# Optimization experiments

Measured on AMD Instinct MI355X. Metric: run time of the kernel, lower is better.

Reference implementation:

```python
import jax, jax.numpy as jnp
import numpy as np

D_MODEL = 1024
D_STATE = 16
D_CONV = 4
EXPAND = 2
D_INNER = D_MODEL * EXPAND


def setup_inputs() -> dict:
    key = jax.random.key(0)
    ks = jax.random.split(key, 10)
    B, L = 2, 2048
    x = jax.random.normal(ks[0], (B, L, D_MODEL), jnp.float32)
    W_in = jax.random.normal(ks[1], (2 * D_INNER, D_MODEL), jnp.float32) * (1.0 / np.sqrt(D_MODEL))
    conv_w = jax.random.normal(ks[2], (D_INNER, 1, D_CONV), jnp.float32) * (1.0 / np.sqrt(D_CONV))
    conv_b = jax.random.normal(ks[3], (D_INNER,), jnp.float32) * 0.1
    W_x = jax.random.normal(ks[4], (2 * D_STATE + 1, D_INNER), jnp.float32) * (1.0 / np.sqrt(D_INNER))
    A_log = jnp.log(jnp.abs(jax.random.normal(ks[5], (D_INNER, D_STATE), jnp.float32)) + 1e-4)
    D_param = jnp.ones((D_INNER,), jnp.float32)
    W_dt = jax.random.normal(ks[6], (D_INNER, 1), jnp.float32)
    b_dt = jax.random.normal(ks[7], (D_INNER,), jnp.float32) * 0.1
    W_out = jax.random.normal(ks[8], (D_MODEL, D_INNER), jnp.float32) * (1.0 / np.sqrt(D_INNER))
    return {"x": x, "W_in": W_in, "conv_w": conv_w, "conv_b": conv_b, "W_x": W_x,
            "A_log": A_log, "D_param": D_param, "W_dt": W_dt, "b_dt": b_dt, "W_out": W_out}


def _forward(x, W_in, conv_w, conv_b, W_x, A_log, D_param, W_dt, b_dt, W_out):
    B, L, _ = x.shape
    xz = x @ W_in.T                                  # [B,L,2*d_inner]
    x_ssm, z = jnp.split(xz, 2, axis=-1)
    # causal depthwise conv: torch pads both sides d_conv-1 then truncates to L == left-pad only
    xc = jnp.transpose(x_ssm, (0, 2, 1))             # [B,d_inner,L]
    xc = jax.lax.conv_general_dilated(
        xc, conv_w, window_strides=(1,), padding=[(D_CONV - 1, 0)],
        feature_group_count=D_INNER, dimension_numbers=("NCH", "OIH", "NCH"))
    xc = xc + conv_b[None, :, None]
    x_ssm = jax.nn.silu(jnp.transpose(xc, (0, 2, 1)))  # [B,L,d_inner]
    proj = x_ssm @ W_x.T                              # [B,L,2*d_state+1]
    B_ssm = proj[..., :D_STATE]                       # [B,L,d_state]
    C_ssm = proj[..., D_STATE:2 * D_STATE]            # [B,L,d_state]
    dt = jax.nn.softplus(proj[..., -1:] * W_dt[:, 0] + b_dt)  # [B,L,d_inner]
    A = -jnp.exp(A_log)                               # [d_inner,d_state]

    def step(h, inp):
        dt_t, Bt, Ct, xt = inp                        # [B,d_inner],[B,n],[B,n],[B,d_inner]
        dA = jnp.exp(dt_t[..., None] * A)             # [B,d_inner,d_state]
        h = dA * h + (xt * dt_t)[..., None] * Bt[:, None, :]
        y = jnp.einsum("bdn,bn->bd", h, Ct)
        return h, y

    h0 = jnp.zeros((B, D_INNER, D_STATE), x.dtype)
    inputs = (jnp.transpose(dt, (1, 0, 2)), jnp.transpose(B_ssm, (1, 0, 2)),
              jnp.transpose(C_ssm, (1, 0, 2)), jnp.transpose(x_ssm, (1, 0, 2)))
    _, ys = jax.lax.scan(step, h0, inputs)            # ys: [L,B,d_inner]
    y = jnp.transpose(ys, (1, 0, 2)) + x_ssm * D_param
    y = y * jax.nn.silu(z)
    return y @ W_out.T


def reference(x, W_in, conv_w, conv_b, W_x, A_log, D_param, W_dt, b_dt, W_out):
    return _forward(x, W_in, conv_w, conv_b, W_x, A_log, D_param, W_dt, b_dt, W_out)
```

## Files before the change

kernel.cpp:

```cpp
#include <hip/hip_runtime.h>
#include <hip/hip_bf16.h>
#include <cstddef>

#define DMODEL 1024
#define DI     2048
#define DS     16
#define LSEQ   2048
#define BATCH  2
#define NC     128
#define TCH    (LSEQ / NC)

typedef __attribute__((ext_vector_type(8))) short short8;
typedef __attribute__((ext_vector_type(4))) float f32x4;
typedef __attribute__((ext_vector_type(2))) float f32x2;
typedef __attribute__((ext_vector_type(8))) unsigned short us8;

__device__ __forceinline__ unsigned short f2bf(float f) {
    unsigned int u = __float_as_uint(f);
    unsigned int r = (u + 0x7fff + ((u >> 16) & 1)) >> 16;
    return (unsigned short)r;
}
__device__ __forceinline__ float bf2f(unsigned short b) {
    return __uint_as_float(((unsigned int)b) << 16);
}

__device__ __forceinline__ float fexp2(float x) {
#if __has_builtin(__builtin_amdgcn_exp2f)
    return __builtin_amdgcn_exp2f(x);
#else
    return exp2f(x);
#endif
}
__device__ __forceinline__ float flog2(float x) {
#if __has_builtin(__builtin_amdgcn_logf)
    return __builtin_amdgcn_logf(x);
#else
    return log2f(x);
#endif
}

#define LOG2E 1.4426950408889634f
#define RLOG2E 0.6931471805599453f

__device__ __forceinline__ float softplus_f(float v) {
    return (v > 20.f) ? v : flog2(1.f + fexp2(v * LOG2E)) * RLOG2E;
}

__device__ __forceinline__ void gload_lds16(const void* g, void* l) {
    __builtin_amdgcn_global_load_lds(
        (const __attribute__((address_space(1))) unsigned int*)g,
        (__attribute__((address_space(3))) unsigned int*)l, 16, 0, 0);
}

__global__ void cvt_bf16(const float* __restrict__ in, unsigned short* __restrict__ out, int n8) {
    int i = blockIdx.x * 256 + threadIdx.x;
    if (i >= n8) return;
    const float4* p = reinterpret_cast<const float4*>(in) + i * 2;
    float4 v0 = p[0], v1 = p[1];
    us8 o;
    o[0] = f2bf(v0.x); o[1] = f2bf(v0.y); o[2] = f2bf(v0.z); o[3] = f2bf(v0.w);
    o[4] = f2bf(v1.x); o[5] = f2bf(v1.y); o[6] = f2bf(v1.z); o[7] = f2bf(v1.w);
    *reinterpret_cast<us8*>(out + (size_t)i * 8) = o;
}

__global__ void prep_wx(const float* __restrict__ wx, unsigned short* __restrict__ out) {
    int i = blockIdx.x * 256 + threadIdx.x;
    if (i >= 48 * 2048 / 8) return;
    size_t o = (size_t)i * 8;
    int row = (int)(o >> 11);
    us8 v;
    if (row < 33) {
        const float4* p = reinterpret_cast<const float4*>(wx + o);
        float4 v0 = p[0], v1 = p[1];
        v[0] = f2bf(v0.x); v[1] = f2bf(v0.y); v[2] = f2bf(v0.z); v[3] = f2bf(v0.w);
        v[4] = f2bf(v1.x); v[5] = f2bf(v1.y); v[6] = f2bf(v1.z); v[7] = f2bf(v1.w);
    } else {
        v = (us8)0;
    }
    *reinterpret_cast<us8*>(out + o) = v;
}

__global__ void prep_A(const float* __restrict__ A_log, float* __restrict__ At2) {
    int i = blockIdx.x * 256 + threadIdx.x;
    if (i >= DS * DI) return;
    int n = i / DI, d = i % DI;
    At2[i] = -__expf(A_log[d * DS + n]) * LOG2E;
}

#define NT1 32
__global__ __launch_bounds__(512, 1)
void gemm1_pipe(const unsigned short* __restrict__ A, const unsigned short* __restrict__ B,
                unsigned short* __restrict__ C) {
    __shared__ unsigned short lds[4][2][256 * 32];

    const int tid = threadIdx.x;
    const int wid = tid >> 6, ln = tid & 63;
    const int wm = wid >> 2, wn = wid & 3;

    int wg = blockIdx.x;
    wg = (wg & 7) * 32 + (wg >> 3);
    const int m0 = (wg >> 4) * 256;
    const int n0 = (wg & 15) * 256;

    const int srow = tid >> 2;
    const int sun  = tid & 3;
    const int ksrc = ((sun ^ ((srow >> 1) & 3)) * 8);

    const int fr = ln & 15;
    const int fku = (ln >> 4);

    f32x4 acc[8][4] = {};

    #define STAGE1(kt)                                                                     \
        do {                                                                               \
            const int bq_ = (kt) & 3;                                                      \
            gload_lds16(A + (size_t)(m0 + srow) * 1024 + (kt) * 32 + ksrc,                 \
                        &lds[bq_][0][srow * 32 + sun * 8]);                                \
            gload_lds16(A + (size_t)(m0 + 128 + srow) * 1024 + (kt) * 32 + ksrc,           \
                        &lds[bq_][0][(128 + srow) * 32 + sun * 8]);                        \
            gload_lds16(B + (size_t)(n0 + srow) * 1024 + (kt) * 32 + ksrc,                 \
                        &lds[bq_][1][srow * 32 + sun * 8]);                                \
            gload_lds16(B + (size_t)(n0 + 128 + srow) * 1024 + (kt) * 32 + ksrc,           \
                        &lds[bq_][1][(128 + srow) * 32 + sun * 8]);                        \
        } while (0)

    STAGE1(0); STAGE1(1); STAGE1(2);
    asm volatile("s_waitcnt vmcnt(8)" ::: "memory");
    __builtin_amdgcn_s_barrier();
    __builtin_amdgcn_sched_barrier(0);

    for (int kt = 0; kt < NT1; ++kt) {
        const int bq = kt & 3;
        if (kt + 3 < NT1) STAGE1(kt + 3);

        short8 af_lo[4], bfr[4], af_hi[4];
        #pragma unroll
        for (int i = 0; i < 4; ++i) {
            int r = wm * 128 + i * 16 + fr;
            int u = fku ^ ((r >> 1) & 3);
            af_lo[i] = *reinterpret_cast<const short8*>(&lds[bq][0][r * 32 + u * 8]);
        }
        #pragma unroll
        for (int j = 0; j < 4; ++j) {
            int r = wn * 64 + j * 16 + fr;
            int u = fku ^ ((r >> 1) & 3);
            bfr[j] = *reinterpret_cast<const short8*>(&lds[bq][1][r * 32 + u * 8]);
        }
        #pragma unroll
        for (int i = 0; i < 4; ++i) {
            int r = wm * 128 + (4 + i) * 16 + fr;
            int u = fku ^ ((r >> 1) & 3);
            af_hi[i] = *reinterpret_cast<const short8*>(&lds[bq][0][r * 32 + u * 8]);
        }
        __builtin_amdgcn_sched_barrier(0);
        __builtin_amdgcn_s_setprio(1);
        #pragma unroll
        for (int i = 0; i < 4; ++i)
            #pragma unroll
            for (int j = 0; j < 4; ++j)
                acc[i][j] = __builtin_amdgcn_mfma_f32_16x16x32_bf16(af_lo[i], bfr[j], acc[i][j], 0, 0, 0);
        __builtin_amdgcn_s_setprio(0);
        __builtin_amdgcn_sched_barrier(0);
        __builtin_amdgcn_s_setprio(1);
        #pragma unroll
        for (int i = 0; i < 4; ++i)
            #pragma unroll
            for (int j = 0; j < 4; ++j)
                acc[4 + i][j] = __builtin_amdgcn_mfma_f32_16x16x32_bf16(af_hi[i], bfr[j], acc[4 + i][j], 0, 0, 0);
        __builtin_amdgcn_s_setprio(0);
        __builtin_amdgcn_sched_barrier(0);

        if (kt < NT1 - 3)       asm volatile("s_waitcnt vmcnt(8)" ::: "memory");
        else if (kt == NT1 - 3) asm volatile("s_waitcnt vmcnt(4)" ::: "memory");
        else if (kt == NT1 - 2) asm volatile("s_waitcnt vmcnt(0)" ::: "memory");
        __builtin_amdgcn_s_barrier();
        __builtin_amdgcn_sched_barrier(0);
    }
    #undef STAGE1

    const int cr = (ln >> 4) * 4, cc = ln & 15;
    #pragma unroll
    for (int i = 0; i < 8; ++i) {
        int row = m0 + wm * 128 + i * 16 + cr;
        #pragma unroll
        for (int j = 0; j < 4; ++j) {
            int col = n0 + wn * 64 + j * 16 + cc;
            #pragma unroll
            for (int r = 0; r < 4; ++r)
                C[(size_t)(row + r) * 4096 + col] = f2bf(acc[i][j][r]);
        }
    }
}

#define NT3 64
__global__ __launch_bounds__(256, 2)
void gemm3_pipe(const unsigned short* __restrict__ A, int lda,
                const unsigned short* __restrict__ B,
                float* __restrict__ C) {
    __shared__ unsigned short As[4][128 * 32];
    __shared__ unsigned short Bs[4][64 * 32];

    const int tid = threadIdx.x;
    const int wid = tid >> 6, ln = tid & 63;
    const int wm = wid >> 1, wn = wid & 1;

    int wg = blockIdx.x;
    wg = (wg & 7) * 64 + (wg >> 3);
    const int m0 = (wg >> 4) * 128;
    const int n0 = (wg & 15) * 64;

    const int srow = tid >> 2;
    const int sun  = tid & 3;
    const int ksrc = ((sun ^ ((srow >> 1) & 3)) * 8);

    const int fr = ln & 15;
    const int fku = (ln >> 4);

    f32x4 acc[4][2] = {};

    #define STAGE3(kt)                                                                     \
        do {                                                                               \
            const int bq_ = (kt) & 3;                                                      \
            gload_lds16(A + (size_t)(m0 + srow) * lda + (kt) * 32 + ksrc,                  \
                        &As[bq_][srow * 32 + sun * 8]);                                    \
            gload_lds16(A + (size_t)(m0 + 64 + srow) * lda + (kt) * 32 + ksrc,             \
                        &As[bq_][(64 + srow) * 32 + sun * 8]);                             \
            gload_lds16(B + (size_t)(n0 + srow) * 2048 + (kt) * 32 + ksrc,                 \
                        &Bs[bq_][srow * 32 + sun * 8]);                                    \
        } while (0)

    STAGE3(0); STAGE3(1); STAGE3(2);
    asm volatile("s_waitcnt vmcnt(6)" ::: "memory");
    __builtin_amdgcn_s_barrier();
    __builtin_amdgcn_sched_barrier(0);

    for (int kt = 0; kt < NT3; ++kt) {
        const int bq = kt & 3;
        if (kt + 3 < NT3) STAGE3(kt + 3);

        short8 af[4], bfr[2];
        #pragma unroll
        for (int i = 0; i < 4; ++i) {
            int r = wm * 64 + i * 16 + fr;
            int u = fku ^ ((r >> 1) & 3);
            af[i] = *reinterpret_cast<const short8*>(&As[bq][r * 32 + u * 8]);
        }
        #pragma unroll
        for (int j = 0; j < 2; ++j) {
            int r = wn * 32 + j * 16 + fr;
            int u = fku ^ ((r >> 1) & 3);
            bfr[j] = *reinterpret_cast<const short8*>(&Bs[bq][r * 32 + u * 8]);
        }
        __builtin_amdgcn_sched_barrier(0);
        __builtin_amdgcn_s_setprio(1);
        #pragma unroll
        for (int i = 0; i < 4; ++i)
            #pragma unroll
            for (int j = 0; j < 2; ++j)
                acc[i][j] = __builtin_amdgcn_mfma_f32_16x16x32_bf16(af[i], bfr[j], acc[i][j], 0, 0, 0);
        __builtin_amdgcn_s_setprio(0);
        __builtin_amdgcn_sched_barrier(0);

        if (kt < NT3 - 3)       asm volatile("s_waitcnt vmcnt(6)" ::: "memory");
        else if (kt == NT3 - 3) asm volatile("s_waitcnt vmcnt(3)" ::: "memory");
        else if (kt == NT3 - 2) asm volatile("s_waitcnt vmcnt(0)" ::: "memory");
        __builtin_amdgcn_s_barrier();
        __builtin_amdgcn_sched_barrier(0);
    }
    #undef STAGE3

    const int cr = (ln >> 4) * 4, cc = ln & 15;
    #pragma unroll
    for (int i = 0; i < 4; ++i) {
        int row = m0 + wm * 64 + i * 16 + cr;
        #pragma unroll
        for (int j = 0; j < 2; ++j) {
            int col = n0 + wn * 32 + j * 16 + cc;
            #pragma unroll
            for (int r = 0; r < 4; ++r)
                C[(size_t)(row + r) * 1024 + col] = acc[i][j][r];
        }
    }
}

__global__ void conv_silu(const unsigned short* __restrict__ xzb, const float* __restrict__ cw,
                          const float* __restrict__ cb, unsigned short* __restrict__ xactb) {
    int i = blockIdx.x * 256 + threadIdx.x;
    if (i >= BATCH * LSEQ * DI / 8) return;
    int d0 = (i % (DI / 8)) * 8;
    int l  = (i / (DI / 8)) % LSEQ;
    int b  = i / ((DI / 8) * LSEQ);

    float4 w[8];
    #pragma unroll
    for (int j = 0; j < 8; ++j)
        w[j] = *reinterpret_cast<const float4*>(cw + (d0 + j) * 4);

    float acc[8];
    #pragma unroll
    for (int j = 0; j < 8; ++j) acc[j] = cb[d0 + j];

    #pragma unroll
    for (int t = 0; t < 4; ++t) {
        int ls = l - 3 + t;
        if (ls >= 0) {
            us8 v = *reinterpret_cast<const us8*>(xzb + (size_t)(b * LSEQ + ls) * 4096 + d0);
            #pragma unroll
            for (int j = 0; j < 8; ++j) {
                float wt = (t == 0) ? w[j].x : (t == 1) ? w[j].y : (t == 2) ? w[j].z : w[j].w;
                acc[j] += bf2f(v[j]) * wt;
            }
        }
    }
    us8 o;
    #pragma unroll
    for (int j = 0; j < 8; ++j) {
        float v = acc[j] / (1.f + __expf(-acc[j]));
        o[j] = f2bf(v);
    }
    *reinterpret_cast<us8*>(xactb + (size_t)i * 8) = o;
}

__global__ __launch_bounds__(256)
void gemm_proj_mfma(const unsigned short* __restrict__ Xb, const unsigned short* __restrict__ Wxb,
                    float* __restrict__ projp) {
    __shared__ unsigned short As[64 * 32];
    __shared__ unsigned short Bs[48 * 32];

    const int tid = threadIdx.x;
    const int wv = tid >> 6, ln = tid & 63;
    const int m0 = blockIdx.x * 64;
    const int kz = blockIdx.y;
    const int srow = tid >> 2, skoff = (tid & 3) * 8;
    const int fr = ln & 15, fk = (ln >> 4) * 8;

    f32x4 acc[3] = {};

    const int k0base = kz * 512;
    for (int k0 = k0base; k0 < k0base + 512; k0 += 32) {
        gload_lds16(Xb + (size_t)(m0 + srow) * DI + k0 + skoff, &As[wv * 512]);
        if (wv < 3)
            gload_lds16(Wxb + (size_t)srow * DI + k0 + skoff, &Bs[wv * 512]);
        __syncthreads();

        short8 af = *reinterpret_cast<const short8*>(&As[(wv * 16 + fr) * 32 + fk]);
        #pragma unroll
        for (int j = 0; j < 3; ++j) {
            short8 bf_ = *reinterpret_cast<const short8*>(&Bs[(j * 16 + fr) * 32 + fk]);
            acc[j] = __builtin_amdgcn_mfma_f32_16x16x32_bf16(af, bf_, acc[j], 0, 0, 0);
        }
        __syncthreads();
    }

    const int cr = (ln >> 4) * 4, cc = ln & 15;
    #pragma unroll
    for (int j = 0; j < 3; ++j) {
        int col = j * 16 + cc;
        if (col < 33) {
            #pragma unroll
            for (int r = 0; r < 4; ++r) {
                int row = m0 + wv * 16 + cr + r;
                projp[(size_t)row * 144 + kz * 36 + col] = acc[j][r];
            }
        }
    }
}

__global__ void proj_combine(const float* __restrict__ projp, float* __restrict__ proj) {
    int idx = blockIdx.x * 256 + threadIdx.x;
    if (idx >= BATCH * LSEQ * 33) return;
    int row = idx / 33, col = idx % 33;
    float s = 0.f;
    #pragma unroll
    for (int kz = 0; kz < 4; ++kz)
        s += projp[(size_t)row * 144 + kz * 36 + col];
    proj[(size_t)row * 36 + col] = s;
}

__global__ __launch_bounds__(256)
void scan_phase1(const unsigned short* __restrict__ xactb, const float* __restrict__ proj,
                 const float* __restrict__ At2, const float* __restrict__ W_dt,
                 const float* __restrict__ b_dt, unsigned short* __restrict__ Hend,
                 float* __restrict__ dtsum, unsigned short* __restrict__ yloc,
                 unsigned short* __restrict__ XZb) {
    const int d = blockIdx.x * 256 + threadIdx.x;
    const int c = blockIdx.y;
    const int b = blockIdx.z;

    f32x2 A2[DS / 2], h2[DS / 2];
    #pragma unroll
    for (int p = 0; p < DS / 2; ++p) {
        A2[p] = (f32x2){At2[(2 * p) * DI + d], At2[(2 * p + 1) * DI + d]};
        h2[p] = (f32x2){0.f, 0.f};
    }
    const float wdt = W_dt[d], bdt = b_dt[d];
    float ssum = 0.f;

    const int l0 = c * TCH;
    #pragma unroll 2
    for (int l = l0; l < l0 + TCH; ++l) {
        const size_t row = (size_t)(b * LSEQ + l);
        const float* pr = proj + row * 36;
        float dt = softplus_f(pr[32] * wdt + bdt);
        ssum += dt;
        XZb[row * 4096 + d] = f2bf(ssum);
        float x = bf2f(xactb[row * DI + d]);
        float xdt = x * dt;
        f32x2 xdt2 = (f32x2){xdt, xdt};
        f32x2 y2 = (f32x2){0.f, 0.f};
        #pragma unroll
        for (int p = 0; p < DS / 2; ++p) {
            f32x2 t = A2[p] * dt;
            f32x2 e2 = (f32x2){fexp2(t.x), fexp2(t.y)};
            h2[p] = e2 * h2[p] + xdt2 * (f32x2){pr[2 * p], pr[2 * p + 1]};
            y2 += h2[p] * (f32x2){pr[16 + 2 * p], pr[17 + 2 * p]};
        }
        yloc[row * DI + d] = f2bf(y2.x + y2.y);
    }
    size_t base = ((size_t)(b * NC + c) * DS) * DI + d;
    #pragma unroll
    for (int p = 0; p < DS / 2; ++p) {
        Hend[base + (size_t)(2 * p) * DI]     = f2bf(h2[p].x);
        Hend[base + (size_t)(2 * p + 1) * DI] = f2bf(h2[p].y);
    }
    dtsum[(size_t)(b * NC + c) * DI + d] = ssum;
}

__global__ void scan_phase2(unsigned short* __restrict__ H, const float* __restrict__ dtsum,
                            const float* __restrict__ At2) {
    int idx = blockIdx.x * 256 + threadIdx.x;
    int b = idx / (DS * DI);
    int r = idx % (DS * DI);
    int n = r / DI, d = r % DI;
    float A2 = At2[n * DI + d];
    float h = 0.f;
    #pragma unroll 4
    for (int c = 0; c < NC; ++c) {
        size_t off = ((size_t)(b * NC + c) * DS + n) * DI + d;
        float He = bf2f(H[off]);
        float P = fexp2(A2 * dtsum[(size_t)(b * NC + c) * DI + d]);
        H[off] = f2bf(h);
        h = P * h + He;
    }
}

__global__ __launch_bounds__(256)
void scan_phase3(const unsigned short* __restrict__ xactb, const unsigned short* __restrict__ yloc,
                 const float* __restrict__ proj, const float* __restrict__ At2,
                 const float* __restrict__ Dp, const unsigned short* __restrict__ Hin,
                 unsigned short* __restrict__ XZb) {
    const int tid = threadIdx.x;
    const int d = blockIdx.x * 256 + tid;
    const int c = blockIdx.y;
    const int b = blockIdx.z;

    f32x2 A2[DS / 2], Hn2[DS / 2];
    size_t hbase = ((size_t)(b * NC + c) * DS) * DI + d;
    #pragma unroll
    for (int p = 0; p < DS / 2; ++p) {
        A2[p]  = (f32x2){At2[(2 * p) * DI + d], At2[(2 * p + 1) * DI + d]};
        Hn2[p] = (f32x2){bf2f(Hin[hbase + (size_t)(2 * p) * DI]),
                         bf2f(Hin[hbase + (size_t)(2 * p + 1) * DI])};
    }

    const float Dv = Dp[d];
    const int l0 = c * TCH;
    #pragma unroll 2
    for (int l = l0; l < l0 + TCH; ++l) {
        const size_t row = (size_t)(b * LSEQ + l);
        const float* pr = proj + row * 36;
        unsigned short* xzrow = XZb + row * 4096;
        float S  = bf2f(xzrow[d]);
        float yl = bf2f(yloc[row * DI + d]);
        float x  = bf2f(xactb[row * DI + d]);
        float z  = bf2f(xzrow[2048 + d]);
        f32x2 corr2 = (f32x2){0.f, 0.f};
        #pragma unroll
        for (int p = 0; p < DS / 2; ++p) {
            f32x2 t = A2[p] * S;
            f32x2 e2 = (f32x2){fexp2(t.x), fexp2(t.y)};
            corr2 += (f32x2){pr[16 + 2 * p], pr[17 + 2 * p]} * e2 * Hn2[p];
        }
        float y = yl + corr2.x + corr2.y + x * Dv;
        float sz = z / (1.f + __expf(-z));
        xzrow[d] = f2bf(y * sz);
    }
}

extern "C" void kernel_launch(void* const* d_in, const int* in_sizes, int n_in,
                              void* d_out, int out_size, void* d_ws, size_t ws_size,
                              hipStream_t stream) {
    const float* x      = (const float*)d_in[0];
    const float* W_in   = (const float*)d_in[1];
    const float* conv_w = (const float*)d_in[2];
    const float* conv_b = (const float*)d_in[3];
    const float* W_x    = (const float*)d_in[4];
    const float* A_log  = (const float*)d_in[5];
    const float* Dp     = (const float*)d_in[6];
    const float* W_dt   = (const float*)d_in[7];
    const float* b_dt   = (const float*)d_in[8];
    const float* W_out  = (const float*)d_in[9];
    float* out = (float*)d_out;

    char* ws = (char*)d_ws;
    unsigned short* XZb   = (unsigned short*)(ws + 0);
    unsigned short* XACTB = (unsigned short*)(ws + 33554432);
    unsigned short* Xb    = (unsigned short*)(ws + 50331648);
    unsigned short* W_inb = (unsigned short*)(ws + 58720256);
    unsigned short* Hbuf  = (unsigned short*)(ws + 67108864);
    unsigned short* YLOC  = (unsigned short*)(ws + 83886080);
    float* PROJ  = (float*)(ws + 100663296);
    float* DTSUM = (float*)(ws + 101711872);
    float* PROJP = (float*)(ws + 103809024);
    float* Abuf  = (float*)(ws + 106954752);
    unsigned short* W_outb = (unsigned short*)(ws + 108003328);
    unsigned short* Wxb48  = (unsigned short*)(ws + 112197632);

    const int M = BATCH * LSEQ;

    cvt_bf16<<<M * DMODEL / 8 / 256, 256, 0, stream>>>(x, Xb, M * DMODEL / 8);
    cvt_bf16<<<2 * DI * DMODEL / 8 / 256, 256, 0, stream>>>(W_in, W_inb, 2 * DI * DMODEL / 8);
    prep_wx<<<48, 256, 0, stream>>>(W_x, Wxb48);
    prep_A<<<DS * DI / 256, 256, 0, stream>>>(A_log, Abuf);

    gemm1_pipe<<<256, 512, 0, stream>>>(Xb, W_inb, XZb);

    conv_silu<<<BATCH * LSEQ * DI / 8 / 256, 256, 0, stream>>>(XZb, conv_w, conv_b, XACTB);

    gemm_proj_mfma<<<dim3(M / 64, 4), 256, 0, stream>>>(XACTB, Wxb48, PROJP);
    proj_combine<<<(M * 33 + 255) / 256, 256, 0, stream>>>(PROJP, PROJ);

    scan_phase1<<<dim3(DI / 256, NC, BATCH), 256, 0, stream>>>(
        XACTB, PROJ, Abuf, W_dt, b_dt, Hbuf, DTSUM, YLOC, XZb);
    scan_phase2<<<BATCH * DS * DI / 256, 256, 0, stream>>>(Hbuf, DTSUM, Abuf);
    scan_phase3<<<dim3(DI / 256, NC, BATCH), 256, 0, stream>>>(
        XACTB, YLOC, PROJ, Abuf, Dp, Hbuf, XZb);

    cvt_bf16<<<DMODEL * DI / 8 / 256, 256, 0, stream>>>(W_out, W_outb, DMODEL * DI / 8);
    gemm3_pipe<<<512, 256, 0, stream>>>(XZb, 4096, W_outb, out);
}
```

Baseline: 211.5 us.

## Fuse prep conversions into one kernel and retile input GEMM to 128x256 tiles

All five small preprocessing launches (x, W_in, W_out, W_x conversions to bf16 and the A transform) are merged into a single prep_all kernel to cut launch overhead. The input projection GEMM moves from 256x256 tiles with a 4-stage LDS pipeline and one block per CU to 128x256 tiles with double buffering, 512 blocks and a launch bound allowing more blocks per CU. The aim is better occupancy and CU coverage in exchange for a shallower prefetch pipeline and less operand reuse per block.

```diff
diff --git a/kernel.cpp b/kernel.cpp
--- a/kernel.cpp
+++ b/kernel.cpp
@@ -52,10 +52,9 @@
         (__attribute__((address_space(3))) unsigned int*)l, 16, 0, 0);
 }
 
-__global__ void cvt_bf16(const float* __restrict__ in, unsigned short* __restrict__ out, int n8) {
-    int i = blockIdx.x * 256 + threadIdx.x;
-    if (i >= n8) return;
-    const float4* p = reinterpret_cast<const float4*>(in) + i * 2;
+__device__ __forceinline__ void cvt8_store(const float* __restrict__ in,
+                                           unsigned short* __restrict__ out, int i) {
+    const float4* p = reinterpret_cast<const float4*>(in) + (size_t)i * 2;
     float4 v0 = p[0], v1 = p[1];
     us8 o;
     o[0] = f2bf(v0.x); o[1] = f2bf(v0.y); o[2] = f2bf(v0.z); o[3] = f2bf(v0.w);
@@ -63,43 +62,51 @@
     *reinterpret_cast<us8*>(out + (size_t)i * 8) = o;
 }
 
-__global__ void prep_wx(const float* __restrict__ wx, unsigned short* __restrict__ out) {
+#define PREP_X   524288
+#define PREP_WI  (PREP_X + 524288)
+#define PREP_WO  (PREP_WI + 262144)
+#define PREP_WX  (PREP_WO + 12288)
+#define PREP_A   (PREP_WX + 32768)
+__global__ void prep_all(const float* __restrict__ x, const float* __restrict__ W_in,
+                         const float* __restrict__ W_out, const float* __restrict__ wx,
+                         const float* __restrict__ A_log,
+                         unsigned short* __restrict__ Xb, unsigned short* __restrict__ W_inb,
+                         unsigned short* __restrict__ W_outb, unsigned short* __restrict__ Wxb48,
+                         float* __restrict__ At2) {
     int i = blockIdx.x * 256 + threadIdx.x;
-    if (i >= 48 * 2048 / 8) return;
-    size_t o = (size_t)i * 8;
-    int row = (int)(o >> 11);
-    us8 v;
-    if (row < 33) {
-        const float4* p = reinterpret_cast<const float4*>(wx + o);
-        float4 v0 = p[0], v1 = p[1];
-        v[0] = f2bf(v0.x); v[1] = f2bf(v0.y); v[2] = f2bf(v0.z); v[3] = f2bf(v0.w);
-        v[4] = f2bf(v1.x); v[5] = f2bf(v1.y); v[6] = f2bf(v1.z); v[7] = f2bf(v1.w);
-    } else {
-        v = (us8)0;
-    }
-    *reinterpret_cast<us8*>(out + o) = v;
-}
-
-__global__ void prep_A(const float* __restrict__ A_log, float* __restrict__ At2) {
-    int i = blockIdx.x * 256 + threadIdx.x;
-    if (i >= DS * DI) return;
-    int n = i / DI, d = i % DI;
-    At2[i] = -__expf(A_log[d * DS + n]) * LOG2E;
-}
-
-#define NT1 32
-__global__ __launch_bounds__(512, 1)
-void gemm1_pipe(const unsigned short* __restrict__ A, const unsigned short* __restrict__ B,
-                unsigned short* __restrict__ C) {
-    __shared__ unsigned short lds[4][2][256 * 32];
+    if (i < PREP_X) {
+        cvt8_store(x, Xb, i);
+    } else if (i < PREP_WI) {
+        cvt8_store(W_in, W_inb, i - PREP_X);
+    } else if (i < PREP_WO) {
+        cvt8_store(W_out, W_outb, i - PREP_WI);
+    } else if (i < PREP_WX) {
+        int j = i - PREP_WO;
+        size_t o = (size_t)j * 8;
+        int row = (int)(o >> 11);
+        if (row < 33) cvt8_store(wx, Wxb48, j);
+        else *reinterpret_cast<us8*>(Wxb48 + o) = (us8)0;
+    } else if (i < PREP_A) {
+        int j = i - PREP_WX;
+        int n = j / DI, d = j % DI;
+        At2[j] = -__expf(A_log[d * DS + n]) * LOG2E;
+    }
+}
+
+#define NTK1 32
+__global__ __launch_bounds__(512, 4)
+void gemm1_2b(const unsigned short* __restrict__ A, const unsigned short* __restrict__ B,
+              unsigned short* __restrict__ C) {
+    __shared__ unsigned short As[2][128 * 32];
+    __shared__ unsigned short Bs[2][256 * 32];
 
     const int tid = threadIdx.x;
     const int wid = tid >> 6, ln = tid & 63;
     const int wm = wid >> 2, wn = wid & 3;
 
     int wg = blockIdx.x;
-    wg = (wg & 7) * 32 + (wg >> 3);
-    const int m0 = (wg >> 4) * 256;
+    wg = (wg & 7) * 64 + (wg >> 3);
+    const int m0 = (wg >> 4) * 128;
     const int n0 = (wg & 15) * 256;
 
     const int srow = tid >> 2;
@@ -109,48 +116,39 @@
     const int fr = ln & 15;
     const int fku = (ln >> 4);
 
-    f32x4 acc[8][4] = {};
-
-    #define STAGE1(kt)                                                                     \
+    f32x4 acc[4][4] = {};
+
+    #define STAGE1(kt, c)                                                                  \
         do {                                                                               \
-            const int bq_ = (kt) & 3;                                                      \
             gload_lds16(A + (size_t)(m0 + srow) * 1024 + (kt) * 32 + ksrc,                 \
-                        &lds[bq_][0][srow * 32 + sun * 8]);                                \
-            gload_lds16(A + (size_t)(m0 + 128 + srow) * 1024 + (kt) * 32 + ksrc,           \
-                        &lds[bq_][0][(128 + srow) * 32 + sun * 8]);                        \
+                        &As[c][srow * 32 + sun * 8]);                                      \
             gload_lds16(B + (size_t)(n0 + srow) * 1024 + (kt) * 32 + ksrc,                 \
-                        &lds[bq_][1][srow * 32 + sun * 8]);                                \
+                        &Bs[c][srow * 32 + sun * 8]);                                      \
             gload_lds16(B + (size_t)(n0 + 128 + srow) * 1024 + (kt) * 32 + ksrc,           \
-                        &lds[bq_][1][(128 + srow) * 32 + sun * 8]);                        \
+                        &Bs[c][(128 + srow) * 32 + sun * 8]);                              \
         } while (0)
 
-    STAGE1(0); STAGE1(1); STAGE1(2);
-    asm volatile("s_waitcnt vmcnt(8)" ::: "memory");
+    STAGE1(0, 0);
+    asm volatile("s_waitcnt vmcnt(0)" ::: "memory");
     __builtin_amdgcn_s_barrier();
     __builtin_amdgcn_sched_barrier(0);
 
-    for (int kt = 0; kt < NT1; ++kt) {
-        const int bq = kt & 3;
-        if (kt + 3 < NT1) STAGE1(kt + 3);
-
-        short8 af_lo[4], bfr[4], af_hi[4];
+    for (int kt = 0; kt < NTK1; ++kt) {
+        const int c = kt & 1;
+        if (kt + 1 < NTK1) STAGE1(kt + 1, c ^ 1);
+
+        short8 af[4], bfr[4];
         #pragma unroll
         for (int i = 0; i < 4; ++i) {
-            int r = wm * 128 + i * 16 + fr;
+            int r = wm * 64 + i * 16 + fr;
             int u = fku ^ ((r >> 1) & 3);
-            af_lo[i] = *reinterpret_cast<const short8*>(&lds[bq][0][r * 32 + u * 8]);
+            af[i] = *reinterpret_cast<const short8*>(&As[c][r * 32 + u * 8]);
         }
         #pragma unroll
         for (int j = 0; j < 4; ++j) {
             int r = wn * 64 + j * 16 + fr;
             int u = fku ^ ((r >> 1) & 3);
-            bfr[j] = *reinterpret_cast<const short8*>(&lds[bq][1][r * 32 + u * 8]);
-        }
-        #pragma unroll
-        for (int i = 0; i < 4; ++i) {
-            int r = wm * 128 + (4 + i) * 16 + fr;
-            int u = fku ^ ((r >> 1) & 3);
-            af_hi[i] = *reinterpret_cast<const short8*>(&lds[bq][0][r * 32 + u * 8]);
+            bfr[j] = *reinterpret_cast<const short8*>(&Bs[c][r * 32 + u * 8]);
         }
         __builtin_amdgcn_sched_barrier(0);
         __builtin_amdgcn_s_setprio(1);
@@ -158,21 +156,11 @@
         for (int i = 0; i < 4; ++i)
             #pragma unroll
             for (int j = 0; j < 4; ++j)
-                acc[i][j] = __builtin_amdgcn_mfma_f32_16x16x32_bf16(af_lo[i], bfr[j], acc[i][j], 0, 0, 0);
+                acc[i][j] = __builtin_amdgcn_mfma_f32_16x16x32_bf16(af[i], bfr[j], acc[i][j], 0, 0, 0);
         __builtin_amdgcn_s_setprio(0);
         __builtin_amdgcn_sched_barrier(0);
-        __builtin_amdgcn_s_setprio(1);
-        #pragma unroll
-        for (int i = 0; i < 4; ++i)
-            #pragma unroll
-            for (int j = 0; j < 4; ++j)
-                acc[4 + i][j] = __builtin_amdgcn_mfma_f32_16x16x32_bf16(af_hi[i], bfr[j], acc[4 + i][j], 0, 0, 0);
-        __builtin_amdgcn_s_setprio(0);
-        __builtin_amdgcn_sched_barrier(0);
-
-        if (kt < NT1 - 3)       asm volatile("s_waitcnt vmcnt(8)" ::: "memory");
-        else if (kt == NT1 - 3) asm volatile("s_waitcnt vmcnt(4)" ::: "memory");
-        else if (kt == NT1 - 2) asm volatile("s_waitcnt vmcnt(0)" ::: "memory");
+
+        if (kt + 1 < NTK1) asm volatile("s_waitcnt vmcnt(0)" ::: "memory");
         __builtin_amdgcn_s_barrier();
         __builtin_amdgcn_sched_barrier(0);
     }
@@ -180,8 +168,8 @@
 
     const int cr = (ln >> 4) * 4, cc = ln & 15;
     #pragma unroll
-    for (int i = 0; i < 8; ++i) {
-        int row = m0 + wm * 128 + i * 16 + cr;
+    for (int i = 0; i < 4; ++i) {
+        int row = m0 + wm * 64 + i * 16 + cr;
         #pragma unroll
         for (int j = 0; j < 4; ++j) {
             int col = n0 + wn * 64 + j * 16 + cc;
@@ -518,12 +506,10 @@
 
     const int M = BATCH * LSEQ;
 
-    cvt_bf16<<<M * DMODEL / 8 / 256, 256, 0, stream>>>(x, Xb, M * DMODEL / 8);
-    cvt_bf16<<<2 * DI * DMODEL / 8 / 256, 256, 0, stream>>>(W_in, W_inb, 2 * DI * DMODEL / 8);
-    prep_wx<<<48, 256, 0, stream>>>(W_x, Wxb48);
-    prep_A<<<DS * DI / 256, 256, 0, stream>>>(A_log, Abuf);
-
-    gemm1_pipe<<<256, 512, 0, stream>>>(Xb, W_inb, XZb);
+    prep_all<<<(PREP_A + 255) / 256, 256, 0, stream>>>(
+        x, W_in, W_out, W_x, A_log, Xb, W_inb, W_outb, Wxb48, Abuf);
+
+    gemm1_2b<<<512, 512, 0, stream>>>(Xb, W_inb, XZb);
 
     conv_silu<<<BATCH * LSEQ * DI / 8 / 256, 256, 0, stream>>>(XZb, conv_w, conv_b, XACTB);
 
@@ -536,6 +522,5 @@
     scan_phase3<<<dim3(DI / 256, NC, BATCH), 256, 0, stream>>>(
         XACTB, YLOC, PROJ, Abuf, Dp, Hbuf, XZb);
 
-    cvt_bf16<<<DMODEL * DI / 8 / 256, 256, 0, stream>>>(W_out, W_outb, DMODEL * DI / 8);
     gemm3_pipe<<<512, 256, 0, stream>>>(XZb, 4096, W_outb, out);
 }
```

Result: faster. 204.8 us (-3.2%).
